# Kernel optimization log

Hardware: AMD Instinct MI355X
Metric: run time of the kernel (lower is better)

## Reference

```python
import jax, jax.numpy as jnp
import numpy as np

N_NODES = 50000
N_EDGES = 500000
L_DIM = 128
MAX_ETYPES = 8
NUM_BASES = 2
K_FRAC = 0.5
SELF_ETYPE = 4  # hardcoded in compute_edge_attention


def setup_inputs() -> dict:
    key = jax.random.key(0)
    ks = jax.random.split(key, 12)
    h = jax.random.normal(ks[0], (N_NODES, L_DIM), dtype=jnp.float32)
    src = jax.random.randint(ks[1], (N_EDGES,), 0, N_NODES, dtype=jnp.int32)
    # ensure no self-loops (the module removes them before attention)
    off = jax.random.randint(ks[2], (N_EDGES,), 1, N_NODES, dtype=jnp.int32)
    dst = (src + off) % N_NODES
    etype = jax.random.randint(ks[3], (N_EDGES,), 0, MAX_ETYPES, dtype=jnp.int32)
    s = 1.0 / np.sqrt(L_DIM)
    W_bases = jax.random.normal(ks[4], (NUM_BASES, 2 * L_DIM, L_DIM), dtype=jnp.float32) * s
    coef = jax.random.normal(ks[5], (MAX_ETYPES, NUM_BASES), dtype=jnp.float32)
    wq_w = jax.random.normal(ks[6], (L_DIM, L_DIM), dtype=jnp.float32) * s
    wq_b = jax.random.normal(ks[7], (L_DIM,), dtype=jnp.float32) * 0.01
    wk_w = jax.random.normal(ks[8], (L_DIM, L_DIM), dtype=jnp.float32) * s
    wk_b = jax.random.normal(ks[9], (L_DIM,), dtype=jnp.float32) * 0.01
    wv_w = jax.random.normal(ks[10], (L_DIM, 1), dtype=jnp.float32) * s
    wv_b = jax.random.normal(ks[11], (1,), dtype=jnp.float32) * 0.01
    return {"h": h, "src": src, "dst": dst, "etype": etype,
            "W_bases": W_bases, "coef": coef,
            "wq_w": wq_w, "wq_b": wq_b, "wk_w": wk_w, "wk_b": wk_b,
            "wv_w": wv_w, "wv_b": wv_b}


def _typed_linear(x, et, W_bases, coef):
    # basis-decomposed typed linear (RGCN-style): W_t = sum_b coef[t,b] * W_b
    xb = jnp.einsum('ei,bio->ebo', x, W_bases)          # [E, B, D]
    return jnp.einsum('ebo,eb->eo', xb, coef[et])        # [E, D]


def reference(h, src, dst, etype, W_bases, coef, wq_w, wq_b, wk_w, wk_b, wv_w, wv_b):
    N, D = h.shape
    scale = jnp.asarray(np.sqrt(D), dtype=h.dtype)

    # self contribution: typed_linear(cat[h,h], etype=4) -> w_v
    self_et = jnp.full((N,), SELF_ETYPE, dtype=jnp.int32)
    self_emb = _typed_linear(jnp.concatenate([h, h], axis=1), self_et, W_bases, coef)
    self_y = self_emb @ wv_w + wv_b                      # [N, 1]

    n_q = h @ wq_w + wq_b                                # [N, D]

    def direction(s_idx, d_idx):
        # per-edge typed linear on concat(src_feat, dst_feat)
        z2 = jnp.concatenate([h[s_idx], h[d_idx]], axis=1)   # [E, 2D]
        emb = _typed_linear(z2, etype, W_bases, coef)        # [E, D]
        n_k = emb @ wk_w + wk_b                              # [E, D]
        n_v = emb @ wv_w + wv_b                              # [E, 1]
        score = jnp.sum(n_k * n_q[d_idx], axis=-1, keepdims=True)
        score = jnp.exp(jnp.clip(score / scale, -10.0, 10.0))  # scaled_exp
        e_val = score * n_v
        wV = jax.ops.segment_sum(e_val, d_idx, num_segments=N)   # [N, 1]
        z = jax.ops.segment_sum(score, d_idx, num_segments=N)    # [N, 1]
        return wV / (z + 1e-6)

    in_y = direction(src, dst)      # original edge direction, aggregate at dst
    out_y = direction(dst, src)     # reversed graph, aggregate at (orig) src
    y = in_y + out_y + self_y       # [N, 1] node attention

    # top-k pooling (single subgraph); dropout is identity in eval mode
    num_keep = max(int(K_FRAC * N), 2)
    _, topk_idx = jax.lax.top_k(y[:, 0], num_keep)
    order = jnp.argsort(topk_idx)
    original_node_ids = topk_idx[order]
    # NOTE: faithful to the source, which indexes h/y with the argsort
    # positions (`sorted_indices`), not the sorted node ids.
    sel = order
    updated_h = h[sel] * jax.nn.sigmoid(y[sel])          # [K, D]
    return original_node_ids, updated_h
```

## Files before the change

kernel.cpp:

```cpp
#include <hip/hip_runtime.h>

#define NN 50000
#define NE 500000
#define DD 128
#define KK 25000
#define NBIN 16384

typedef unsigned short u16;
typedef __attribute__((ext_vector_type(8))) unsigned short u16x8;

__device__ inline u16 f2bf(float x) {
  unsigned u = __float_as_uint(x);
  unsigned r = (u + 0x7FFFu + ((u >> 16) & 1u)) >> 16;
  return (u16)r;
}
__device__ inline float bf2f(u16 b) {
  return __uint_as_float(((unsigned)b) << 16);
}

__global__ void k_zero(float* zf, int nf, int* zi, int ni) {
  int i = blockIdx.x * blockDim.x + threadIdx.x;
  int stride = gridDim.x * blockDim.x;
  for (int k = i; k < nf; k += stride) zf[k] = 0.0f;
  for (int k = i; k < ni; k += stride) zi[k] = 0;
}

__global__ void k_smallmats(const float* __restrict__ Wb, const float* __restrict__ wkw,
                            const float* __restrict__ wvw, float* Ck0, float* Ck1,
                            float* Dk0, float* Dk1, float* vecs) {
  int b = blockIdx.x, tid = threadIdx.x;
  if (b < 64) {
    int mat = b >> 4;
    int basis = mat & 1;
    int rowoff = (mat >> 1) * DD;
    float* outp = (mat == 0) ? Ck0 : ((mat == 1) ? Ck1 : ((mat == 2) ? Dk0 : Dk1));
    int i = (b & 15) * 2 + (tid >> 7);
    int t = tid & 127;
    const float* wrow = Wb + (size_t)(basis * 2 * DD + rowoff + i) * DD;
    float s = 0.0f;
    for (int m = 0; m < DD; m++) s += wrow[m] * wkw[m * DD + t];
    outp[i * DD + t] = s;
  } else if (b < 68) {
    int which = b - 64;
    int basis = which & 1, rowoff = (which >> 1) * DD;
    if (tid < DD) {
      const float* wrow = Wb + (size_t)(basis * 2 * DD + rowoff + tid) * DD;
      float s = 0.0f;
      for (int m = 0; m < DD; m++) s += wrow[m] * wvw[m];
      vecs[which * DD + tid] = s;
    }
  }
}

#define NPB 16
__global__ void __launch_bounds__(256) k_nodeA(
    const float* __restrict__ h, const float* __restrict__ Mq,
    const float* __restrict__ C0, const float* __restrict__ C1,
    const float* __restrict__ D0, const float* __restrict__ D1,
    const float* __restrict__ wqb, const float* __restrict__ wkb,
    const float* __restrict__ vecs, const float* __restrict__ coef,
    const float* __restrict__ wvb, u16* __restrict__ pkq,
    float* __restrict__ t0o, float* __restrict__ t1o, float* __restrict__ uo,
    float* __restrict__ av0o, float* __restrict__ av1o, float* __restrict__ bv0o,
    float* __restrict__ bv1o, float* __restrict__ selfyo) {
  __shared__ float hs[NPB * DD];
  __shared__ float red[4][8][7];
  int tid = threadIdx.x;
  int n0 = blockIdx.x * NPB;
  for (int idx = tid; idx < NPB * DD; idx += 256) {
    int n = n0 + (idx >> 7);
    hs[idx] = (n < NN) ? h[(size_t)n * DD + (idx & 127)] : 0.0f;
  }
  __syncthreads();
  int col = tid & 127, half = tid >> 7;
  int lane = tid & 63, wid = tid >> 6;
  float aq[8], ap0[8], ap1[8], ad0[8], ad1[8];
#pragma unroll
  for (int j = 0; j < 8; j++) { aq[j] = 0.f; ap0[j] = 0.f; ap1[j] = 0.f; ad0[j] = 0.f; ad1[j] = 0.f; }
  for (int k4 = 0; k4 < DD / 4; k4++) {
    float q0 = Mq[(4 * k4 + 0) * DD + col], q1 = Mq[(4 * k4 + 1) * DD + col];
    float q2 = Mq[(4 * k4 + 2) * DD + col], q3 = Mq[(4 * k4 + 3) * DD + col];
    float c00 = C0[(4 * k4 + 0) * DD + col], c01 = C0[(4 * k4 + 1) * DD + col];
    float c02 = C0[(4 * k4 + 2) * DD + col], c03 = C0[(4 * k4 + 3) * DD + col];
    float c10 = C1[(4 * k4 + 0) * DD + col], c11 = C1[(4 * k4 + 1) * DD + col];
    float c12 = C1[(4 * k4 + 2) * DD + col], c13 = C1[(4 * k4 + 3) * DD + col];
    float d00 = D0[(4 * k4 + 0) * DD + col], d01 = D0[(4 * k4 + 1) * DD + col];
    float d02 = D0[(4 * k4 + 2) * DD + col], d03 = D0[(4 * k4 + 3) * DD + col];
    float d10 = D1[(4 * k4 + 0) * DD + col], d11 = D1[(4 * k4 + 1) * DD + col];
    float d12 = D1[(4 * k4 + 2) * DD + col], d13 = D1[(4 * k4 + 3) * DD + col];
#pragma unroll
    for (int j = 0; j < 8; j++) {
      const float4 hv = *(const float4*)&hs[(half * 8 + j) * DD + 4 * k4];
      aq[j] += hv.x * q0 + hv.y * q1 + hv.z * q2 + hv.w * q3;
      ap0[j] += hv.x * c00 + hv.y * c01 + hv.z * c02 + hv.w * c03;
      ap1[j] += hv.x * c10 + hv.y * c11 + hv.z * c12 + hv.w * c13;
      ad0[j] += hv.x * d00 + hv.y * d01 + hv.z * d02 + hv.w * d03;
      ad1[j] += hv.x * d10 + hv.y * d11 + hv.z * d12 + hv.w * d13;
    }
  }
  float bias = wqb[col];
  float wkbc = wkb[col];
  float va0 = vecs[col], va1 = vecs[DD + col], vb0 = vecs[2 * DD + col],
        vb1 = vecs[3 * DD + col];
#pragma unroll
  for (int j = 0; j < 8; j++) {
    int n = n0 + half * 8 + j;
    float qv = aq[j] + bias;
    float hc = hs[(half * 8 + j) * DD + col];
    if (n < NN) {
      ushort2 st;
      st.x = f2bf(ap0[j]);
      st.y = f2bf(ap1[j]);
      *(ushort2*)&pkq[(size_t)n * 384 + 2 * col] = st;
      pkq[(size_t)n * 384 + 256 + col] = f2bf(qv);
    }
    float v0 = ad0[j] * qv;
    float v1 = ad1[j] * qv;
    float vu = qv * wkbc;
    float a0 = hc * va0, a1 = hc * va1, b0 = hc * vb0, b1 = hc * vb1;
#pragma unroll
    for (int off = 32; off; off >>= 1) {
      v0 += __shfl_xor(v0, off);
      v1 += __shfl_xor(v1, off);
      vu += __shfl_xor(vu, off);
      a0 += __shfl_xor(a0, off);
      a1 += __shfl_xor(a1, off);
      b0 += __shfl_xor(b0, off);
      b1 += __shfl_xor(b1, off);
    }
    if (lane == 0) {
      red[wid][j][0] = v0; red[wid][j][1] = v1; red[wid][j][2] = vu;
      red[wid][j][3] = a0; red[wid][j][4] = a1; red[wid][j][5] = b0;
      red[wid][j][6] = b1;
    }
  }
  __syncthreads();
  if (tid < 16) {
    int j = tid & 7, g = tid >> 3;
    int n = n0 + g * 8 + j;
    if (n < NN) {
      int w0 = 2 * g, w1 = 2 * g + 1;
      float t0 = red[w0][j][0] + red[w1][j][0];
      float t1 = red[w0][j][1] + red[w1][j][1];
      float uu = red[w0][j][2] + red[w1][j][2];
      float a0 = red[w0][j][3] + red[w1][j][3];
      float a1 = red[w0][j][4] + red[w1][j][4];
      float b0 = red[w0][j][5] + red[w1][j][5];
      float b1 = red[w0][j][6] + red[w1][j][6];
      t0o[n] = t0; t1o[n] = t1; uo[n] = uu;
      av0o[n] = a0; av1o[n] = a1; bv0o[n] = b0; bv1o[n] = b1;
      float c40 = coef[4 * 2 + 0], c41 = coef[4 * 2 + 1];
      selfyo[n] = c40 * (a0 + b0) + c41 * (a1 + b1) + wvb[0];
    }
  }
}

__global__ void __launch_bounds__(256) k_edges16(
    const int* __restrict__ src, const int* __restrict__ dst,
    const int* __restrict__ et, const float* __restrict__ coef,
    const float* __restrict__ wvb, const u16* __restrict__ pkq,
    const float* __restrict__ t0, const float* __restrict__ t1,
    const float* __restrict__ u, const float* __restrict__ av0,
    const float* __restrict__ av1, const float* __restrict__ bv0,
    const float* __restrict__ bv1, float* wvin, float* zin, float* wvout,
    float* zout) {
  int tid = threadIdx.x;
  int sub = tid & 15;
  int g = tid >> 4;
  long e = (long)blockIdx.x * 16 + g;
  int s = src[e], d = dst[e], t = et[e];
  float c0 = coef[t * 2], c1 = coef[t * 2 + 1];
  const u16* rs = pkq + (size_t)s * 384;
  const u16* rd = pkq + (size_t)d * 384;
  u16x8 ps0 = *(const u16x8*)(rs + sub * 16);
  u16x8 ps1 = *(const u16x8*)(rs + sub * 16 + 8);
  u16x8 pd0 = *(const u16x8*)(rd + sub * 16);
  u16x8 pd1 = *(const u16x8*)(rd + sub * 16 + 8);
  u16x8 qs = *(const u16x8*)(rs + 256 + sub * 8);
  u16x8 qd = *(const u16x8*)(rd + 256 + sub * 8);
  float df = 0.0f, dr = 0.0f;
#pragma unroll
  for (int k = 0; k < 4; k++) {
    df += (c0 * bf2f(ps0[2 * k]) + c1 * bf2f(ps0[2 * k + 1])) * bf2f(qd[k]);
    dr += (c0 * bf2f(pd0[2 * k]) + c1 * bf2f(pd0[2 * k + 1])) * bf2f(qs[k]);
    df += (c0 * bf2f(ps1[2 * k]) + c1 * bf2f(ps1[2 * k + 1])) * bf2f(qd[4 + k]);
    dr += (c0 * bf2f(pd1[2 * k]) + c1 * bf2f(pd1[2 * k + 1])) * bf2f(qs[4 + k]);
  }
#pragma unroll
  for (int off = 8; off; off >>= 1) {
    df += __shfl_xor(df, off);
    dr += __shfl_xor(dr, off);
  }
  if (sub == 0) {
    const float scale = 11.3137084989847604f;
    float wvbd = wvb[0];
    float sf = (df + c0 * t0[d] + c1 * t1[d] + u[d]) / scale;
    sf = fminf(fmaxf(sf, -10.0f), 10.0f);
    float ef = expf(sf);
    float nvf = c0 * (av0[s] + bv0[d]) + c1 * (av1[s] + bv1[d]) + wvbd;
    atomicAdd(&wvin[d], ef * nvf);
    atomicAdd(&zin[d], ef);
    float sr = (dr + c0 * t0[s] + c1 * t1[s] + u[s]) / scale;
    sr = fminf(fmaxf(sr, -10.0f), 10.0f);
    float er = expf(sr);
    float nvr = c0 * (av0[d] + bv0[s]) + c1 * (av1[d] + bv1[s]) + wvbd;
    atomicAdd(&wvout[s], er * nvr);
    atomicAdd(&zout[s], er);
  }
}

__device__ inline unsigned fkey(float f) {
  unsigned b = __float_as_uint(f);
  return (b & 0x80000000u) ? ~b : (b | 0x80000000u);
}

__global__ void k_y(const float* wvin, const float* zin, const float* wvout,
                    const float* zout, const float* selfy, float* y, unsigned* ykey,
                    int* hist) {
  int n = blockIdx.x * blockDim.x + threadIdx.x;
  if (n < NN) {
    float v = wvin[n] / (zin[n] + 1e-6f) + wvout[n] / (zout[n] + 1e-6f) + selfy[n];
    y[n] = v;
    unsigned k = fkey(v);
    ykey[n] = k;
    atomicAdd(&hist[k >> 18], 1);
  }
}

__global__ void k_hsum(const int* __restrict__ hist, int* __restrict__ bsum) {
  __shared__ int sh[256];
  int t = threadIdx.x;
  sh[t] = hist[blockIdx.x * 256 + t];
  __syncthreads();
  for (int off = 128; off; off >>= 1) {
    if (t < off) sh[t] += sh[t + off];
    __syncthreads();
  }
  if (t == 0) bsum[blockIdx.x] = sh[0];
}

__global__ void k_hfinal(const int* __restrict__ hist, const int* __restrict__ bsum,
                         int* __restrict__ suff) {
  __shared__ int sh[256];
  __shared__ int carry;
  int t = threadIdx.x;
  int bx = blockIdx.x;
  if (t < 64) {
    int m = (t > bx) ? bsum[t] : 0;
#pragma unroll
    for (int off = 32; off; off >>= 1) m += __shfl_xor(m, off);
    if (t == 0) carry = m;
  }
  int base = bx * 256;
  int own = hist[base + 255 - t];
  sh[t] = own;
  __syncthreads();
  for (int off = 1; off < 256; off <<= 1) {
    int v = (t >= off) ? sh[t - off] : 0;
    __syncthreads();
    sh[t] += v;
    __syncthreads();
  }
  suff[base + 255 - t] = carry + sh[t] - own;
}

__global__ void k_scatmem(const unsigned* __restrict__ ykey, const int* __restrict__ suff,
                          int* __restrict__ cur, int* __restrict__ binlist) {
  int i = blockIdx.x * 256 + threadIdx.x;
  if (i >= NN) return;
  int b = ykey[i] >> 18;
  int slot = suff[b] + atomicAdd(&cur[b], 1);
  binlist[slot] = i;
}

__global__ void k_rankbin(const unsigned* __restrict__ ykey, const int* __restrict__ suff,
                          const int* __restrict__ hist, const int* __restrict__ binlist,
                          int* __restrict__ rank) {
  int i = blockIdx.x * 256 + threadIdx.x;
  if (i >= NN) return;
  unsigned ki = ykey[i];
  int b = ki >> 18;
  int base = suff[b];
  int end = base + hist[b];
  int cnt = 0;
  for (int s = base; s < end; s++) {
    int j = binlist[s];
    unsigned kj = ykey[j];
    cnt += (kj > ki || (kj == ki && j < i)) ? 1 : 0;
  }
  rank[i] = base + cnt;
}

__global__ void k_bcnt(const int* rank, int* bcnt) {
  __shared__ int sh[256];
  int i = blockIdx.x * 256 + threadIdx.x;
  int f = (i < NN && rank[i] < KK) ? 1 : 0;
  sh[threadIdx.x] = f;
  __syncthreads();
  for (int off = 128; off; off >>= 1) {
    if (threadIdx.x < off) sh[threadIdx.x] += sh[threadIdx.x + off];
    __syncthreads();
  }
  if (threadIdx.x == 0) bcnt[blockIdx.x] = sh[0];
}

__global__ void k_scan(int* bcnt, int nb) {
  __shared__ int sh[256];
  int t = threadIdx.x;
  int v = (t < nb) ? bcnt[t] : 0;
  sh[t] = v;
  __syncthreads();
  for (int off = 1; off < 256; off <<= 1) {
    int u2 = (t >= off) ? sh[t - off] : 0;
    __syncthreads();
    sh[t] += u2;
    __syncthreads();
  }
  if (t < nb) bcnt[t] = sh[t] - v;
}

__global__ void k_scatter(const int* rank, const int* bcnt, const float* y,
                          float* out_ids, int* selp, float* sig) {
  __shared__ int sh[256];
  int i = blockIdx.x * 256 + threadIdx.x;
  int f = (i < NN && rank[i] < KK) ? 1 : 0;
  sh[threadIdx.x] = f;
  __syncthreads();
  for (int off = 1; off < 256; off <<= 1) {
    int v = (threadIdx.x >= off) ? sh[threadIdx.x - off] : 0;
    __syncthreads();
    sh[threadIdx.x] += v;
    __syncthreads();
  }
  if (f) {
    int slot = bcnt[blockIdx.x] + sh[threadIdx.x] - 1;
    out_ids[slot] = (float)i;
    int p = rank[i];
    selp[slot] = p;
    sig[slot] = 1.0f / (1.0f + expf(-y[p]));
  }
}

__global__ void k_outh(const float* h, const int* selp, const float* sig, float* out) {
  long idx = (long)blockIdx.x * 256 + threadIdx.x;
  if (idx >= (long)KK * DD) return;
  int slot = (int)(idx >> 7), c = (int)(idx & 127);
  int p = selp[slot];
  out[KK + idx] = h[(size_t)p * DD + c] * sig[slot];
}

extern "C" void kernel_launch(void* const* d_in, const int* in_sizes, int n_in,
                              void* d_out, int out_size, void* d_ws, size_t ws_size,
                              hipStream_t stream) {
  const float* h = (const float*)d_in[0];
  const int* src = (const int*)d_in[1];
  const int* dst = (const int*)d_in[2];
  const int* etype = (const int*)d_in[3];
  const float* Wb = (const float*)d_in[4];
  const float* coef = (const float*)d_in[5];
  const float* wqw = (const float*)d_in[6];
  const float* wqb = (const float*)d_in[7];
  const float* wkw = (const float*)d_in[8];
  const float* wkb = (const float*)d_in[9];
  const float* wvw = (const float*)d_in[10];
  const float* wvb = (const float*)d_in[11];
  float* out = (float*)d_out;

  float* W = (float*)d_ws;
  size_t o = 0;
  u16* PKQ = (u16*)(W + o); o += (size_t)NN * 192;
  float* Ck0 = W + o;  o += DD * DD;
  float* Ck1 = W + o;  o += DD * DD;
  float* Dk0 = W + o;  o += DD * DD;
  float* Dk1 = W + o;  o += DD * DD;
  float* vecs = W + o; o += 4 * DD;
  float* t0 = W + o;   o += NN;
  float* t1 = W + o;   o += NN;
  float* av0 = W + o;  o += NN;
  float* av1 = W + o;  o += NN;
  float* bv0 = W + o;  o += NN;
  float* bv1 = W + o;  o += NN;
  float* u = W + o;    o += NN;
  float* selfy = W + o; o += NN;
  float* wvin = W + o;  o += NN;
  float* zin = W + o;   o += NN;
  float* wvout = W + o; o += NN;
  float* zout = W + o;  o += NN;
  float* y = W + o;     o += NN;
  unsigned* ykey = (unsigned*)(W + o); o += NN;
  float* sig = W + o;   o += KK;
  int* ibase = (int*)(W + o);
  int* rank = ibase;
  int* bcnt = ibase + NN;
  int* selp = ibase + NN + 256;
  int* hist = ibase + 2 * NN + 256;
  int* cur = hist + NBIN;
  int* suff = cur + NBIN;
  int* bsum = suff + NBIN;
  int* binlist = bsum + 64;

  int nb = (NN + 255) / 256;

  k_zero<<<256, 256, 0, stream>>>(wvin, 4 * NN, hist, 2 * NBIN);
  k_smallmats<<<68, 256, 0, stream>>>(Wb, wkw, wvw, Ck0, Ck1, Dk0, Dk1, vecs);
  k_nodeA<<<(NN + NPB - 1) / NPB, 256, 0, stream>>>(
      h, wqw, Ck0, Ck1, Dk0, Dk1, wqb, wkb, vecs, coef, wvb, PKQ, t0, t1, u,
      av0, av1, bv0, bv1, selfy);
  k_edges16<<<NE / 16, 256, 0, stream>>>(src, dst, etype, coef, wvb, PKQ, t0, t1, u,
                                         av0, av1, bv0, bv1, wvin, zin, wvout, zout);
  k_y<<<nb, 256, 0, stream>>>(wvin, zin, wvout, zout, selfy, y, ykey, hist);
  k_hsum<<<64, 256, 0, stream>>>(hist, bsum);
  k_hfinal<<<64, 256, 0, stream>>>(hist, bsum, suff);
  k_scatmem<<<nb, 256, 0, stream>>>(ykey, suff, cur, binlist);
  k_rankbin<<<nb, 256, 0, stream>>>(ykey, suff, hist, binlist, rank);
  k_bcnt<<<nb, 256, 0, stream>>>(rank, bcnt);
  k_scan<<<1, 256, 0, stream>>>(bcnt, nb);
  k_scatter<<<nb, 256, 0, stream>>>(rank, bcnt, y, out, selp, sig);
  k_outh<<<(KK * DD) / 256, 256, 0, stream>>>(h, selp, sig, out);
}
```

Before: 517.1 us.

## Use MFMA f16 matrix cores for per-node projections and switch packed storage to fp16

Replaces the scalar FP32 per-node projection kernel with an MFMA 16x16x32 f16 kernel that computes q, the two key-projection matrices and the two t-matrices as one 32x640 product per block, using weights pre-swizzled into fragment layout by a rewritten small-matrix kernel. The packed node table changes from bf16 to fp16, with a plain non-interleaved layout that the edge kernel now reads. The goal is to cut the FP32 ALU cost of the node stage. The cost is lower input precision for h and the weights, which are converted to fp16, and this could flip a few top-k selections near ties.

```diff
diff --git a/kernel.cpp b/kernel.cpp
--- a/kernel.cpp
+++ b/kernel.cpp
@@ -5,18 +5,11 @@
 #define DD 128
 #define KK 25000
 #define NBIN 16384
-
-typedef unsigned short u16;
-typedef __attribute__((ext_vector_type(8))) unsigned short u16x8;
-
-__device__ inline u16 f2bf(float x) {
-  unsigned u = __float_as_uint(x);
-  unsigned r = (u + 0x7FFFu + ((u >> 16) & 1u)) >> 16;
-  return (u16)r;
-}
-__device__ inline float bf2f(u16 b) {
-  return __uint_as_float(((unsigned)b) << 16);
-}
+#define HP 136
+
+typedef _Float16 f16;
+typedef __attribute__((ext_vector_type(8))) _Float16 f16x8;
+typedef __attribute__((ext_vector_type(4))) float f32x4;
 
 __global__ void k_zero(float* zf, int nf, int* zi, int ni) {
   int i = blockIdx.x * blockDim.x + threadIdx.x;
@@ -25,129 +18,170 @@
   for (int k = i; k < ni; k += stride) zi[k] = 0;
 }
 
-__global__ void k_smallmats(const float* __restrict__ Wb, const float* __restrict__ wkw,
-                            const float* __restrict__ wvw, float* Ck0, float* Ck1,
-                            float* Dk0, float* Dk1, float* vecs) {
-  int b = blockIdx.x, tid = threadIdx.x;
-  if (b < 64) {
-    int mat = b >> 4;
-    int basis = mat & 1;
-    int rowoff = (mat >> 1) * DD;
-    float* outp = (mat == 0) ? Ck0 : ((mat == 1) ? Ck1 : ((mat == 2) ? Dk0 : Dk1));
-    int i = (b & 15) * 2 + (tid >> 7);
-    int t = tid & 127;
+__global__ void k_smallmats2(const float* __restrict__ Wb, const float* __restrict__ wqw,
+                             const float* __restrict__ wkw, const float* __restrict__ wvw,
+                             f16* __restrict__ Wcs, float* __restrict__ vecs) {
+  int idx = blockIdx.x * 256 + threadIdx.x;
+  if (idx < 640 * 128) {
+    int gcol = idx >> 7, k = idx & 127;
+    float val;
+    if (gcol < 128) {
+      val = wqw[k * DD + gcol];
+    } else {
+      int part = (gcol - 128) >> 7;
+      int c = (gcol - 128) & 127;
+      int basis = part & 1;
+      int rowoff = (part >> 1) * DD;
+      const float* wrow = Wb + (size_t)(basis * 2 * DD + rowoff + k) * DD;
+      float s = 0.f;
+      for (int m = 0; m < DD; m++) s += wrow[m] * wkw[m * DD + c];
+      val = s;
+    }
+    int ct = gcol >> 4, cl = gcol & 15, kc = k >> 5, kr = k & 31;
+    int lane = (kr >> 3) * 16 + cl, e = kr & 7;
+    Wcs[(size_t)(((ct * 4 + kc) * 64 + lane) * 8 + e)] = (f16)val;
+  } else if (idx < 640 * 128 + 512) {
+    int j = idx - 640 * 128;
+    int which = j >> 7, i = j & 127;
+    int basis = which & 1, rowoff = (which >> 1) * DD;
     const float* wrow = Wb + (size_t)(basis * 2 * DD + rowoff + i) * DD;
-    float s = 0.0f;
-    for (int m = 0; m < DD; m++) s += wrow[m] * wkw[m * DD + t];
-    outp[i * DD + t] = s;
-  } else if (b < 68) {
-    int which = b - 64;
-    int basis = which & 1, rowoff = (which >> 1) * DD;
-    if (tid < DD) {
-      const float* wrow = Wb + (size_t)(basis * 2 * DD + rowoff + tid) * DD;
-      float s = 0.0f;
-      for (int m = 0; m < DD; m++) s += wrow[m] * wvw[m];
-      vecs[which * DD + tid] = s;
-    }
-  }
-}
-
-#define NPB 16
-__global__ void __launch_bounds__(256) k_nodeA(
-    const float* __restrict__ h, const float* __restrict__ Mq,
-    const float* __restrict__ C0, const float* __restrict__ C1,
-    const float* __restrict__ D0, const float* __restrict__ D1,
+    float s = 0.f;
+    for (int m = 0; m < DD; m++) s += wrow[m] * wvw[m];
+    vecs[j] = s;
+  }
+}
+
+__global__ void __launch_bounds__(256) k_nodeMM(
+    const float* __restrict__ h, const f16* __restrict__ Wcs,
     const float* __restrict__ wqb, const float* __restrict__ wkb,
     const float* __restrict__ vecs, const float* __restrict__ coef,
-    const float* __restrict__ wvb, u16* __restrict__ pkq,
-    float* __restrict__ t0o, float* __restrict__ t1o, float* __restrict__ uo,
-    float* __restrict__ av0o, float* __restrict__ av1o, float* __restrict__ bv0o,
-    float* __restrict__ bv1o, float* __restrict__ selfyo) {
-  __shared__ float hs[NPB * DD];
-  __shared__ float red[4][8][7];
+    const float* __restrict__ wvb, f16* __restrict__ pkq, float* __restrict__ t0o,
+    float* __restrict__ t1o, float* __restrict__ uo, float* __restrict__ av0o,
+    float* __restrict__ av1o, float* __restrict__ bv0o, float* __restrict__ bv1o,
+    float* __restrict__ selfyo) {
+  __shared__ f16 hsF[32 * HP];
+  __shared__ float qL[32][132];
   int tid = threadIdx.x;
-  int n0 = blockIdx.x * NPB;
-  for (int idx = tid; idx < NPB * DD; idx += 256) {
-    int n = n0 + (idx >> 7);
-    hs[idx] = (n < NN) ? h[(size_t)n * DD + (idx & 127)] : 0.0f;
-  }
-  __syncthreads();
-  int col = tid & 127, half = tid >> 7;
+  int n0 = blockIdx.x * 32;
+  for (int idx = tid; idx < 32 * DD; idx += 256) {
+    int r = idx >> 7, c = idx & 127;
+    int n = n0 + r;
+    float v = (n < NN) ? h[(size_t)n * DD + c] : 0.f;
+    hsF[r * HP + c] = (f16)v;
+  }
+  __syncthreads();
   int lane = tid & 63, wid = tid >> 6;
-  float aq[8], ap0[8], ap1[8], ad0[8], ad1[8];
-#pragma unroll
-  for (int j = 0; j < 8; j++) { aq[j] = 0.f; ap0[j] = 0.f; ap1[j] = 0.f; ad0[j] = 0.f; ad1[j] = 0.f; }
-  for (int k4 = 0; k4 < DD / 4; k4++) {
-    float q0 = Mq[(4 * k4 + 0) * DD + col], q1 = Mq[(4 * k4 + 1) * DD + col];
-    float q2 = Mq[(4 * k4 + 2) * DD + col], q3 = Mq[(4 * k4 + 3) * DD + col];
-    float c00 = C0[(4 * k4 + 0) * DD + col], c01 = C0[(4 * k4 + 1) * DD + col];
-    float c02 = C0[(4 * k4 + 2) * DD + col], c03 = C0[(4 * k4 + 3) * DD + col];
-    float c10 = C1[(4 * k4 + 0) * DD + col], c11 = C1[(4 * k4 + 1) * DD + col];
-    float c12 = C1[(4 * k4 + 2) * DD + col], c13 = C1[(4 * k4 + 3) * DD + col];
-    float d00 = D0[(4 * k4 + 0) * DD + col], d01 = D0[(4 * k4 + 1) * DD + col];
-    float d02 = D0[(4 * k4 + 2) * DD + col], d03 = D0[(4 * k4 + 3) * DD + col];
-    float d10 = D1[(4 * k4 + 0) * DD + col], d11 = D1[(4 * k4 + 1) * DD + col];
-    float d12 = D1[(4 * k4 + 2) * DD + col], d13 = D1[(4 * k4 + 3) * DD + col];
-#pragma unroll
-    for (int j = 0; j < 8; j++) {
-      const float4 hv = *(const float4*)&hs[(half * 8 + j) * DD + 4 * k4];
-      aq[j] += hv.x * q0 + hv.y * q1 + hv.z * q2 + hv.w * q3;
-      ap0[j] += hv.x * c00 + hv.y * c01 + hv.z * c02 + hv.w * c03;
-      ap1[j] += hv.x * c10 + hv.y * c11 + hv.z * c12 + hv.w * c13;
-      ad0[j] += hv.x * d00 + hv.y * d01 + hv.z * d02 + hv.w * d03;
-      ad1[j] += hv.x * d10 + hv.y * d11 + hv.z * d12 + hv.w * d13;
-    }
-  }
-  float bias = wqb[col];
-  float wkbc = wkb[col];
-  float va0 = vecs[col], va1 = vecs[DD + col], vb0 = vecs[2 * DD + col],
-        vb1 = vecs[3 * DD + col];
-#pragma unroll
-  for (int j = 0; j < 8; j++) {
-    int n = n0 + half * 8 + j;
-    float qv = aq[j] + bias;
-    float hc = hs[(half * 8 + j) * DD + col];
+  int nh = wid & 1;
+  int ctb = (wid >> 1) * 20;
+  int cl = lane & 15, kq = lane >> 4;
+  int base_node = 16 * nh;
+
+  f16x8 afr[4];
+#pragma unroll
+  for (int kc = 0; kc < 4; kc++)
+    afr[kc] = *(const f16x8*)&hsF[(base_node + cl) * HP + kc * 32 + kq * 8];
+
+  f32x4 acc[20];
+#pragma unroll
+  for (int t = 0; t < 20; t++) acc[t] = (f32x4){0.f, 0.f, 0.f, 0.f};
+
+  const f16x8* Wf = (const f16x8*)Wcs;
+#pragma unroll
+  for (int t = 0; t < 20; t++) {
+    int ct = ctb + t;
+#pragma unroll
+    for (int kc = 0; kc < 4; kc++) {
+      f16x8 bfr = Wf[(ct * 4 + kc) * 64 + lane];
+      acc[t] = __builtin_amdgcn_mfma_f32_16x16x32_f16(afr[kc], bfr, acc[t], 0, 0, 0);
+    }
+  }
+
+  float upart[4] = {0.f, 0.f, 0.f, 0.f};
+#pragma unroll
+  for (int t = 0; t < 20; t++) {
+    int ct = ctb + t;
+    int gc = ct * 16 + cl;
+    if (ct < 8) {
+      float wq = wqb[gc], wk = wkb[gc];
+#pragma unroll
+      for (int r = 0; r < 4; r++) {
+        int row = base_node + kq * 4 + r;
+        float qv = acc[t][r] + wq;
+        qL[row][gc] = qv;
+        int n = n0 + row;
+        if (n < NN) pkq[(size_t)n * 384 + 256 + gc] = (f16)qv;
+        upart[r] += wk * qv;
+      }
+    } else if (ct < 16) {
+#pragma unroll
+      for (int r = 0; r < 4; r++) {
+        int n = n0 + base_node + kq * 4 + r;
+        if (n < NN) pkq[(size_t)n * 384 + (gc - 128)] = (f16)acc[t][r];
+      }
+    } else if (ct < 24) {
+#pragma unroll
+      for (int r = 0; r < 4; r++) {
+        int n = n0 + base_node + kq * 4 + r;
+        if (n < NN) pkq[(size_t)n * 384 + 128 + (gc - 256)] = (f16)acc[t][r];
+      }
+    }
+  }
+  if (ctb == 0) {
+#pragma unroll
+    for (int r = 0; r < 4; r++) {
+#pragma unroll
+      for (int off = 1; off < 16; off <<= 1) upart[r] += __shfl_xor(upart[r], off);
+      int n = n0 + base_node + kq * 4 + r;
+      if (cl == 0 && n < NN) uo[n] = upart[r];
+    }
+  }
+  __syncthreads();
+  if (ctb == 20) {
+    float tp0[4] = {0.f, 0.f, 0.f, 0.f}, tp1[4] = {0.f, 0.f, 0.f, 0.f};
+#pragma unroll
+    for (int t = 0; t < 20; t++) {
+      int ct = ctb + t;
+      int gc = ct * 16 + cl;
+      if (ct >= 24 && ct < 32) {
+#pragma unroll
+        for (int r = 0; r < 4; r++)
+          tp0[r] += acc[t][r] * qL[base_node + kq * 4 + r][gc - 384];
+      } else if (ct >= 32) {
+#pragma unroll
+        for (int r = 0; r < 4; r++)
+          tp1[r] += acc[t][r] * qL[base_node + kq * 4 + r][gc - 512];
+      }
+    }
+#pragma unroll
+    for (int r = 0; r < 4; r++) {
+#pragma unroll
+      for (int off = 1; off < 16; off <<= 1) {
+        tp0[r] += __shfl_xor(tp0[r], off);
+        tp1[r] += __shfl_xor(tp1[r], off);
+      }
+      int n = n0 + base_node + kq * 4 + r;
+      if (cl == 0 && n < NN) { t0o[n] = tp0[r]; t1o[n] = tp1[r]; }
+    }
+  }
+  int nn2 = tid >> 3, sub = tid & 7;
+  float a0 = 0.f, a1 = 0.f, b0 = 0.f, b1 = 0.f;
+  for (int c = sub * 16; c < sub * 16 + 16; c++) {
+    float hv = (float)hsF[nn2 * HP + c];
+    a0 += hv * vecs[c];
+    a1 += hv * vecs[DD + c];
+    b0 += hv * vecs[2 * DD + c];
+    b1 += hv * vecs[3 * DD + c];
+  }
+#pragma unroll
+  for (int off = 1; off < 8; off <<= 1) {
+    a0 += __shfl_xor(a0, off);
+    a1 += __shfl_xor(a1, off);
+    b0 += __shfl_xor(b0, off);
+    b1 += __shfl_xor(b1, off);
+  }
+  if (sub == 0) {
+    int n = n0 + nn2;
     if (n < NN) {
-      ushort2 st;
-      st.x = f2bf(ap0[j]);
-      st.y = f2bf(ap1[j]);
-      *(ushort2*)&pkq[(size_t)n * 384 + 2 * col] = st;
-      pkq[(size_t)n * 384 + 256 + col] = f2bf(qv);
-    }
-    float v0 = ad0[j] * qv;
-    float v1 = ad1[j] * qv;
-    float vu = qv * wkbc;
-    float a0 = hc * va0, a1 = hc * va1, b0 = hc * vb0, b1 = hc * vb1;
-#pragma unroll
-    for (int off = 32; off; off >>= 1) {
-      v0 += __shfl_xor(v0, off);
-      v1 += __shfl_xor(v1, off);
-      vu += __shfl_xor(vu, off);
-      a0 += __shfl_xor(a0, off);
-      a1 += __shfl_xor(a1, off);
-      b0 += __shfl_xor(b0, off);
-      b1 += __shfl_xor(b1, off);
-    }
-    if (lane == 0) {
-      red[wid][j][0] = v0; red[wid][j][1] = v1; red[wid][j][2] = vu;
-      red[wid][j][3] = a0; red[wid][j][4] = a1; red[wid][j][5] = b0;
-      red[wid][j][6] = b1;
-    }
-  }
-  __syncthreads();
-  if (tid < 16) {
-    int j = tid & 7, g = tid >> 3;
-    int n = n0 + g * 8 + j;
-    if (n < NN) {
-      int w0 = 2 * g, w1 = 2 * g + 1;
-      float t0 = red[w0][j][0] + red[w1][j][0];
-      float t1 = red[w0][j][1] + red[w1][j][1];
-      float uu = red[w0][j][2] + red[w1][j][2];
-      float a0 = red[w0][j][3] + red[w1][j][3];
-      float a1 = red[w0][j][4] + red[w1][j][4];
-      float b0 = red[w0][j][5] + red[w1][j][5];
-      float b1 = red[w0][j][6] + red[w1][j][6];
-      t0o[n] = t0; t1o[n] = t1; uo[n] = uu;
       av0o[n] = a0; av1o[n] = a1; bv0o[n] = b0; bv1o[n] = b1;
       float c40 = coef[4 * 2 + 0], c41 = coef[4 * 2 + 1];
       selfyo[n] = c40 * (a0 + b0) + c41 * (a1 + b1) + wvb[0];
@@ -158,7 +192,7 @@
 __global__ void __launch_bounds__(256) k_edges16(
     const int* __restrict__ src, const int* __restrict__ dst,
     const int* __restrict__ et, const float* __restrict__ coef,
-    const float* __restrict__ wvb, const u16* __restrict__ pkq,
+    const float* __restrict__ wvb, const f16* __restrict__ pkq,
     const float* __restrict__ t0, const float* __restrict__ t1,
     const float* __restrict__ u, const float* __restrict__ av0,
     const float* __restrict__ av1, const float* __restrict__ bv0,
@@ -170,21 +204,19 @@
   long e = (long)blockIdx.x * 16 + g;
   int s = src[e], d = dst[e], t = et[e];
   float c0 = coef[t * 2], c1 = coef[t * 2 + 1];
-  const u16* rs = pkq + (size_t)s * 384;
-  const u16* rd = pkq + (size_t)d * 384;
-  u16x8 ps0 = *(const u16x8*)(rs + sub * 16);
-  u16x8 ps1 = *(const u16x8*)(rs + sub * 16 + 8);
-  u16x8 pd0 = *(const u16x8*)(rd + sub * 16);
-  u16x8 pd1 = *(const u16x8*)(rd + sub * 16 + 8);
-  u16x8 qs = *(const u16x8*)(rs + 256 + sub * 8);
-  u16x8 qd = *(const u16x8*)(rd + 256 + sub * 8);
-  float df = 0.0f, dr = 0.0f;
-#pragma unroll
-  for (int k = 0; k < 4; k++) {
-    df += (c0 * bf2f(ps0[2 * k]) + c1 * bf2f(ps0[2 * k + 1])) * bf2f(qd[k]);
-    dr += (c0 * bf2f(pd0[2 * k]) + c1 * bf2f(pd0[2 * k + 1])) * bf2f(qs[k]);
-    df += (c0 * bf2f(ps1[2 * k]) + c1 * bf2f(ps1[2 * k + 1])) * bf2f(qd[4 + k]);
-    dr += (c0 * bf2f(pd1[2 * k]) + c1 * bf2f(pd1[2 * k + 1])) * bf2f(qs[4 + k]);
+  const f16* rs = pkq + (size_t)s * 384;
+  const f16* rd = pkq + (size_t)d * 384;
+  f16x8 p0s = *(const f16x8*)(rs + sub * 8);
+  f16x8 p1s = *(const f16x8*)(rs + 128 + sub * 8);
+  f16x8 qse = *(const f16x8*)(rs + 256 + sub * 8);
+  f16x8 p0d = *(const f16x8*)(rd + sub * 8);
+  f16x8 p1d = *(const f16x8*)(rd + 128 + sub * 8);
+  f16x8 qde = *(const f16x8*)(rd + 256 + sub * 8);
+  float df = 0.f, dr = 0.f;
+#pragma unroll
+  for (int j = 0; j < 8; j++) {
+    df += (c0 * (float)p0s[j] + c1 * (float)p1s[j]) * (float)qde[j];
+    dr += (c0 * (float)p0d[j] + c1 * (float)p1d[j]) * (float)qse[j];
   }
 #pragma unroll
   for (int off = 8; off; off >>= 1) {
@@ -368,12 +400,9 @@
 
   float* W = (float*)d_ws;
   size_t o = 0;
-  u16* PKQ = (u16*)(W + o); o += (size_t)NN * 192;
-  float* Ck0 = W + o;  o += DD * DD;
-  float* Ck1 = W + o;  o += DD * DD;
-  float* Dk0 = W + o;  o += DD * DD;
-  float* Dk1 = W + o;  o += DD * DD;
-  float* vecs = W + o; o += 4 * DD;
+  f16* PKQ = (f16*)(W + o); o += (size_t)NN * 192;
+  f16* Wcs = (f16*)(W + o); o += 40960;
+  float* vecs = W + o; o += 512;
   float* t0 = W + o;   o += NN;
   float* t1 = W + o;   o += NN;
   float* av0 = W + o;  o += NN;
@@ -402,10 +431,10 @@
   int nb = (NN + 255) / 256;
 
   k_zero<<<256, 256, 0, stream>>>(wvin, 4 * NN, hist, 2 * NBIN);
-  k_smallmats<<<68, 256, 0, stream>>>(Wb, wkw, wvw, Ck0, Ck1, Dk0, Dk1, vecs);
-  k_nodeA<<<(NN + NPB - 1) / NPB, 256, 0, stream>>>(
-      h, wqw, Ck0, Ck1, Dk0, Dk1, wqb, wkb, vecs, coef, wvb, PKQ, t0, t1, u,
-      av0, av1, bv0, bv1, selfy);
+  k_smallmats2<<<(640 * 128 + 512 + 255) / 256, 256, 0, stream>>>(Wb, wqw, wkw, wvw,
+                                                                  Wcs, vecs);
+  k_nodeMM<<<(NN + 31) / 32, 256, 0, stream>>>(h, Wcs, wqb, wkb, vecs, coef, wvb, PKQ,
+                                               t0, t1, u, av0, av1, bv0, bv1, selfy);
   k_edges16<<<NE / 16, 256, 0, stream>>>(src, dst, etype, coef, wvb, PKQ, t0, t1, u,
                                          av0, av1, bv0, bv1, wvin, zin, wvout, zout);
   k_y<<<nb, 256, 0, stream>>>(wvin, zin, wvout, zout, selfy, y, ykey, hist);
```

Measured after the change: 494.6 us. 1.05x faster.
